# Kernel optimization log

Hardware: AMD Instinct MI355X
Metric: run time of the kernel (lower is better)

Reference implementation:

```python
import jax, jax.numpy as jnp
import numpy as np

MAX_DISP = 4  # matches init_kwargs


def setup_inputs() -> dict:
    key = jax.random.key(0)
    k1, k2 = jax.random.split(key)
    fmap1 = jax.random.normal(k1, (8, 256, 64, 128), dtype=jnp.float32)
    fmap2 = jax.random.normal(k2, (8, 256, 64, 128), dtype=jnp.float32)
    return {"fmap1": fmap1, "fmap2": fmap2}


def reference(fmap1, fmap2):
    # corr(x,y,dx,dy) = sum_c fmap1[c,y,x] * fmap2[c,y+dy,x+dx]
    pad = MAX_DISP
    B, C, H, W = fmap1.shape
    f2p = jnp.pad(fmap2, ((0, 0), (0, 0), (pad, pad), (pad, pad)))
    side = 2 * pad + 1  # 9 -> 81 displacements total
    # Loop over the small fixed set of 81 static displacements; each term is a
    # fused elementwise-multiply + channel reduction (einsum over c).
    corrs = [
        jnp.einsum('bchw,bchw->bhw', fmap1, f2p[:, :, y0:y0 + H, x0:x0 + W])
        for y0 in range(side)
        for x0 in range(side)
    ]
    return jnp.stack(corrs, axis=1)  # (B, 81, H, W)
```

## Files before the change

kernel.cpp:

```cpp
#include <hip/hip_runtime.h>


namespace {
constexpr int B_ = 8, C_ = 256, H_ = 64, W_ = 128;
constexpr int SIDE = 9, ND = 81, PAD = 4;
constexpr int HW = H_ * W_;
constexpr int KC = 32, NCH = C_ / KC;
constexpr int YB = 8, RWS = YB + 2 * PAD;
constexpr int XB = 16;
constexpr int NQ = 4;
constexpr int YP_ = H_ + 2 * PAD;
constexpr int XP_ = 144;
constexpr size_t ROWU = (size_t)NQ * XP_;
constexpr size_t PERB = (size_t)NCH * YP_ * ROWU;
constexpr size_t NW2 = (size_t)B_ * PERB;
constexpr size_t WS_BYTES = NW2 * 16;
constexpr int TILE_U4 = RWS * NQ * 32;
}

typedef __attribute__((ext_vector_type(8))) short short8;
typedef __attribute__((ext_vector_type(4))) float float4v;
typedef __attribute__((address_space(1))) void gvoid;
typedef __attribute__((address_space(3))) void svoid;

__device__ __forceinline__ unsigned bf16rne(float f) {
  unsigned u = __float_as_uint(f);
  return (u + 0x7fffu + ((u >> 16) & 1u)) >> 16;
}
__device__ __forceinline__ unsigned packbf2(float lo, float hi) {
  return bf16rne(lo) | (bf16rne(hi) << 16);
}

__global__ __launch_bounds__(256)
void cvt_f2(const float* __restrict__ f2, uint4* __restrict__ w2) {
  const int id = blockIdx.x;
  const int b = id & 7;
  const int e = (id >> 3) * 256 + (int)threadIdx.x;
  const int xp = e % XP_;
  int r = e / XP_;
  const int q = r & 3;
  r >>= 2;
  const int yp = r % YP_;
  const int cs = r / YP_;
  const int yg = yp - PAD, xg = xp - PAD;
  uint4 o = {0u, 0u, 0u, 0u};
  if (yg >= 0 && yg < H_ && xg >= 0 && xg < W_) {
    const float* s = f2 + ((size_t)(b * C_ + cs * KC + q * 8) * H_ + yg) * W_ + xg;
    o.x = packbf2(s[0 * HW], s[1 * HW]);
    o.y = packbf2(s[2 * HW], s[3 * HW]);
    o.z = packbf2(s[4 * HW], s[5 * HW]);
    o.w = packbf2(s[6 * HW], s[7 * HW]);
  }
  w2[(size_t)b * PERB + e] = o;
}

__global__ __launch_bounds__(512, 4)
void corr_mfma2(const float* __restrict__ f1, const uint4* __restrict__ w2,
                float* __restrict__ out) {
  __shared__ uint4 f2s[2 * TILE_U4];

  const int id = blockIdx.x;
  const int b = id & 7;
  const int k = id >> 3;
  const int xg = k & 7, yg = k >> 3;
  const int x0 = xg * XB, y0 = yg * YB;

  const int t = threadIdx.x, lane = t & 63, w = t >> 6;
  const int v = lane & 15, q = lane >> 4;
  const int sq = q << 1;
  const int l_hi = lane >> 5;
  const int l_xq = lane & 31;

  const uint4* w2b = w2 + (size_t)b * PERB;
  const float* f1b = f1 + (size_t)b * C_ * HW;

  auto issue_stage = [&](int ch, int buf) {
    const uint4* wc = w2b + (size_t)ch * ((size_t)YP_ * ROWU);
#pragma unroll
    for (int kk = 0; kk < 4; ++kk) {
      const int r = 2 * w + (kk >> 1);
      const int qp = kk & 1;
      const int qq = 2 * qp + l_hi;
      const int xqs = l_xq ^ (qq << 1);
      const uint4* gp = wc + (size_t)(y0 + r) * ROWU + (size_t)qq * XP_ + x0 + xqs;
      uint4* lp = &f2s[buf * TILE_U4 + (r * NQ + qp * 2) * 32];
      __builtin_amdgcn_global_load_lds((gvoid*)gp, (svoid*)lp, 16, 0, 0);
    }
  };
  auto issue_f1 = [&](int ch, float* p) {
    const float* fp =
        f1b + ((size_t)(ch * KC + q * 8) * H_ + (y0 + w)) * W_ + x0 + v;
#pragma unroll
    for (int j = 0; j < 8; ++j) p[j] = fp[(size_t)j * HW];
  };

  float4v acc[SIDE][2];
#pragma unroll
  for (int i = 0; i < SIDE; ++i) {
    acc[i][0] = (float4v){0.f, 0.f, 0.f, 0.f};
    acc[i][1] = (float4v){0.f, 0.f, 0.f, 0.f};
  }

  float p0[8], p1[8];
  issue_stage(0, 0);
  __builtin_amdgcn_sched_barrier(0);
  issue_f1(0, p0);
  __builtin_amdgcn_sched_barrier(0);
  issue_stage(1, 1);
  __builtin_amdgcn_sched_barrier(0);

#pragma unroll
  for (int ch = 0; ch < NCH; ++ch) {
    float* pc = (ch & 1) ? p1 : p0;
    uint4 afu;
    afu.x = packbf2(pc[0], pc[1]);
    afu.y = packbf2(pc[2], pc[3]);
    afu.z = packbf2(pc[4], pc[5]);
    afu.w = packbf2(pc[6], pc[7]);
    const short8 af = __builtin_bit_cast(short8, afu);

    asm volatile("s_waitcnt vmcnt(4)" ::: "memory");
    __builtin_amdgcn_s_barrier();
    __builtin_amdgcn_sched_barrier(0);

    if (ch + 1 < NCH) issue_f1(ch + 1, (ch & 1) ? p0 : p1);

    const int bo = (ch & 1) * TILE_U4;
#pragma unroll
    for (int dy = 0; dy < SIDE; ++dy) {
      const uint4* base = &f2s[bo + ((w + dy) * NQ + q) * 32];
      const short8 b0 = __builtin_bit_cast(short8, base[v ^ sq]);
      const short8 b1 = __builtin_bit_cast(short8, base[(v + 16) ^ sq]);
      acc[dy][0] =
          __builtin_amdgcn_mfma_f32_16x16x32_bf16(af, b0, acc[dy][0], 0, 0, 0);
      acc[dy][1] =
          __builtin_amdgcn_mfma_f32_16x16x32_bf16(af, b1, acc[dy][1], 0, 0, 0);
    }
    __builtin_amdgcn_sched_barrier(0);
    __builtin_amdgcn_s_barrier();
    __builtin_amdgcn_sched_barrier(0);
    if (ch + 2 < NCH) issue_stage(ch + 2, ch & 1);
  }

  const int y = y0 + w;
  float* outb = out + (size_t)b * ND * HW + (size_t)y * W_ + x0;
#pragma unroll
  for (int dy = 0; dy < SIDE; ++dy) {
#pragma unroll
    for (int r = 0; r < 4; ++r) {
      const int m = q * 4 + r;
      const int dx0 = v - m;
      if (dx0 >= 0 && dx0 <= 8)
        outb[(size_t)(dy * SIDE + dx0) * HW + m] = acc[dy][0][r];
      const int dx1 = v - m + 16;
      if (dx1 <= 8)
        outb[(size_t)(dy * SIDE + dx1) * HW + m] = acc[dy][1][r];
    }
  }
}

namespace fb {
constexpr int PXS = 20, F2PX = 32, F2U = 16 * (F2PX / 4) * 16;
}

__global__ __launch_bounds__(512, 4)
void corr_fb(const float* __restrict__ f1, const float* __restrict__ f2,
             float* __restrict__ out) {
  using namespace fb;
  __shared__ __align__(16) unsigned f2s[RWS * F2PX * PXS];
  __shared__ __align__(16) unsigned f1s[YB * XB * PXS];

  const int id = blockIdx.x;
  const int b = id & 7;
  const int k = id >> 3;
  const int xg = k & 7, yg = k >> 3;
  const int x0 = xg * XB, y0 = yg * YB;
  const int t = threadIdx.x, lane = t & 63, w = t >> 6;
  const int v = lane & 15, q = lane >> 4;

  float4v acc[SIDE][2];
#pragma unroll
  for (int i = 0; i < SIDE; ++i) {
    acc[i][0] = (float4v){0.f, 0.f, 0.f, 0.f};
    acc[i][1] = (float4v){0.f, 0.f, 0.f, 0.f};
  }
  const float* __restrict__ f1b = f1 + (size_t)b * C_ * HW;
  const float* __restrict__ f2b = f2 + (size_t)b * C_ * HW;

  for (int ch = 0; ch < NCH; ++ch) {
    const int c0 = ch * KC;
    if (ch) __syncthreads();
#pragma unroll
    for (int u0 = 0; u0 < F2U; u0 += 512) {
      const int u = u0 + t;
      const int cp = u & 15;
      const int t2 = u >> 4;
      const int pxq = t2 & 7;
      const int r = t2 >> 3;
      const int ygl = y0 - PAD + r;
      const int xb = x0 - PAD + pxq * 4;
      float4 va = make_float4(0.f, 0.f, 0.f, 0.f), vb = va;
      if (ygl >= 0 && ygl < H_ && xb >= 0 && xb <= W_ - 4) {
        const float* p = f2b + ((size_t)(c0 + 2 * cp) * H_ + ygl) * W_ + xb;
        va = *(const float4*)p;
        vb = *(const float4*)(p + HW);
      }
      unsigned* d = &f2s[(r * F2PX + pxq * 4) * PXS + cp];
      d[0 * PXS] = packbf2(va.x, vb.x);
      d[1 * PXS] = packbf2(va.y, vb.y);
      d[2 * PXS] = packbf2(va.z, vb.z);
      d[3 * PXS] = packbf2(va.w, vb.w);
    }
    {
      const int cp = t & 15;
      const int t2 = t >> 4;
      const int pxq = t2 & 3;
      const int r = t2 >> 2;
      const float* p =
          f1b + ((size_t)(c0 + 2 * cp) * H_ + (y0 + r)) * W_ + x0 + pxq * 4;
      const float4 va = *(const float4*)p;
      const float4 vb = *(const float4*)(p + HW);
      unsigned* d = &f1s[(r * XB + pxq * 4) * PXS + cp];
      d[0 * PXS] = packbf2(va.x, vb.x);
      d[1 * PXS] = packbf2(va.y, vb.y);
      d[2 * PXS] = packbf2(va.z, vb.z);
      d[3 * PXS] = packbf2(va.w, vb.w);
    }
    __syncthreads();

    const short8 af = __builtin_bit_cast(
        short8, *(const uint4*)&f1s[(w * XB + v) * PXS + 4 * q]);
#pragma unroll
    for (int dy = 0; dy < SIDE; ++dy) {
      const unsigned* fp = &f2s[((w + dy) * F2PX + v) * PXS + 4 * q];
      const short8 b0 = __builtin_bit_cast(short8, *(const uint4*)fp);
      const short8 b1 =
          __builtin_bit_cast(short8, *(const uint4*)(fp + 16 * PXS));
      acc[dy][0] =
          __builtin_amdgcn_mfma_f32_16x16x32_bf16(af, b0, acc[dy][0], 0, 0, 0);
      acc[dy][1] =
          __builtin_amdgcn_mfma_f32_16x16x32_bf16(af, b1, acc[dy][1], 0, 0, 0);
    }
  }
  const int y = y0 + w;
  float* outb = out + (size_t)b * ND * HW + (size_t)y * W_ + x0;
#pragma unroll
  for (int dy = 0; dy < SIDE; ++dy) {
#pragma unroll
    for (int r = 0; r < 4; ++r) {
      const int m = q * 4 + r;
      const int dx0 = v - m;
      if (dx0 >= 0 && dx0 <= 8)
        outb[(size_t)(dy * SIDE + dx0) * HW + m] = acc[dy][0][r];
      const int dx1 = v - m + 16;
      if (dx1 <= 8)
        outb[(size_t)(dy * SIDE + dx1) * HW + m] = acc[dy][1][r];
    }
  }
}

extern "C" void kernel_launch(void* const* d_in, const int* in_sizes, int n_in,
                              void* d_out, int out_size, void* d_ws,
                              size_t ws_size, hipStream_t stream) {
  (void)in_sizes; (void)n_in; (void)out_size;
  const float* f1 = (const float*)d_in[0];
  const float* f2 = (const float*)d_in[1];
  float* out = (float*)d_out;
  if (ws_size >= WS_BYTES) {
    uint4* w2 = (uint4*)d_ws;
    cvt_f2<<<dim3((unsigned)(NW2 / 256)), 256, 0, stream>>>(f2, w2);
    corr_mfma2<<<dim3(512), 512, 0, stream>>>(f1, w2, out);
  } else {
    corr_fb<<<dim3(512), 512, 0, stream>>>(f1, f2, out);
  }
}
```

Measured before the change: 182.6 us.

## Deepen fmap1 prefetch to triple buffer and vectorize bf16 conversion kernel

The conversion kernel now handles two x positions per thread, using float2 loads and writing two uint4 outputs, and launches half as many blocks. The main MFMA kernel prefetches fmap1 two chunks ahead with a three-slot register buffer. The waitcnt is relaxed to match the extra loads in flight, and wave priority is raised around the MFMA loop. The aim is to hide global-load latency for fmap1 and cut conversion-kernel instruction overhead, at the cost of more registers and possible occupancy pressure.

```diff
diff --git a/kernel.cpp b/kernel.cpp
--- a/kernel.cpp
+++ b/kernel.cpp
@@ -35,23 +35,36 @@
 void cvt_f2(const float* __restrict__ f2, uint4* __restrict__ w2) {
   const int id = blockIdx.x;
   const int b = id & 7;
-  const int e = (id >> 3) * 256 + (int)threadIdx.x;
-  const int xp = e % XP_;
-  int r = e / XP_;
+  const int e2 = (id >> 3) * 256 + (int)threadIdx.x;
+  const int xp2 = e2 % (XP_ / 2);
+  int r = e2 / (XP_ / 2);
   const int q = r & 3;
   r >>= 2;
   const int yp = r % YP_;
   const int cs = r / YP_;
+  const int xp = 2 * xp2;
   const int yg = yp - PAD, xg = xp - PAD;
-  uint4 o = {0u, 0u, 0u, 0u};
-  if (yg >= 0 && yg < H_ && xg >= 0 && xg < W_) {
-    const float* s = f2 + ((size_t)(b * C_ + cs * KC + q * 8) * H_ + yg) * W_ + xg;
-    o.x = packbf2(s[0 * HW], s[1 * HW]);
-    o.y = packbf2(s[2 * HW], s[3 * HW]);
-    o.z = packbf2(s[4 * HW], s[5 * HW]);
-    o.w = packbf2(s[6 * HW], s[7 * HW]);
-  }
-  w2[(size_t)b * PERB + e] = o;
+  uint4 o0 = {0u, 0u, 0u, 0u}, o1 = o0;
+  if (yg >= 0 && yg < H_ && xg >= 0 && xg <= W_ - 2) {
+    const float* s =
+        f2 + ((size_t)(b * C_ + cs * KC + q * 8) * H_ + yg) * W_ + xg;
+    const float2 v0 = *(const float2*)(s + 0 * HW);
+    const float2 v1 = *(const float2*)(s + 1 * HW);
+    const float2 v2 = *(const float2*)(s + 2 * HW);
+    const float2 v3 = *(const float2*)(s + 3 * HW);
+    const float2 v4 = *(const float2*)(s + 4 * HW);
+    const float2 v5 = *(const float2*)(s + 5 * HW);
+    const float2 v6 = *(const float2*)(s + 6 * HW);
+    const float2 v7 = *(const float2*)(s + 7 * HW);
+    o0.x = packbf2(v0.x, v1.x);  o1.x = packbf2(v0.y, v1.y);
+    o0.y = packbf2(v2.x, v3.x);  o1.y = packbf2(v2.y, v3.y);
+    o0.z = packbf2(v4.x, v5.x);  o1.z = packbf2(v4.y, v5.y);
+    o0.w = packbf2(v6.x, v7.x);  o1.w = packbf2(v6.y, v7.y);
+  }
+  const size_t e = (((size_t)(cs * YP_ + yp) * NQ + q) * XP_) + xp;
+  uint4* d = w2 + (size_t)b * PERB + e;
+  d[0] = o0;
+  d[1] = o1;
 }
 
 __global__ __launch_bounds__(512, 4)
@@ -101,17 +114,19 @@
     acc[i][1] = (float4v){0.f, 0.f, 0.f, 0.f};
   }
 
-  float p0[8], p1[8];
+  float pbuf[3][8];
   issue_stage(0, 0);
   __builtin_amdgcn_sched_barrier(0);
-  issue_f1(0, p0);
+  issue_f1(0, pbuf[0]);
   __builtin_amdgcn_sched_barrier(0);
   issue_stage(1, 1);
   __builtin_amdgcn_sched_barrier(0);
+  issue_f1(1, pbuf[1]);
+  __builtin_amdgcn_sched_barrier(0);
 
 #pragma unroll
   for (int ch = 0; ch < NCH; ++ch) {
-    float* pc = (ch & 1) ? p1 : p0;
+    float* pc = pbuf[ch % 3];
     uint4 afu;
     afu.x = packbf2(pc[0], pc[1]);
     afu.y = packbf2(pc[2], pc[3]);
@@ -119,13 +134,13 @@
     afu.w = packbf2(pc[6], pc[7]);
     const short8 af = __builtin_bit_cast(short8, afu);
 
-    asm volatile("s_waitcnt vmcnt(4)" ::: "memory");
+    asm volatile("s_waitcnt vmcnt(12)" ::: "memory");
+    __builtin_amdgcn_sched_barrier(0);
     __builtin_amdgcn_s_barrier();
     __builtin_amdgcn_sched_barrier(0);
 
-    if (ch + 1 < NCH) issue_f1(ch + 1, (ch & 1) ? p0 : p1);
-
     const int bo = (ch & 1) * TILE_U4;
+    __builtin_amdgcn_s_setprio(1);
 #pragma unroll
     for (int dy = 0; dy < SIDE; ++dy) {
       const uint4* base = &f2s[bo + ((w + dy) * NQ + q) * 32];
@@ -136,10 +151,16 @@
       acc[dy][1] =
           __builtin_amdgcn_mfma_f32_16x16x32_bf16(af, b1, acc[dy][1], 0, 0, 0);
     }
+    __builtin_amdgcn_s_setprio(0);
     __builtin_amdgcn_sched_barrier(0);
     __builtin_amdgcn_s_barrier();
     __builtin_amdgcn_sched_barrier(0);
-    if (ch + 2 < NCH) issue_stage(ch + 2, ch & 1);
+    if (ch + 2 < NCH) {
+      issue_stage(ch + 2, ch & 1);
+      __builtin_amdgcn_sched_barrier(0);
+      issue_f1(ch + 2, pbuf[(ch + 2) % 3]);
+      __builtin_amdgcn_sched_barrier(0);
+    }
   }
 
   const int y = y0 + w;
@@ -268,7 +289,7 @@
   float* out = (float*)d_out;
   if (ws_size >= WS_BYTES) {
     uint4* w2 = (uint4*)d_ws;
-    cvt_f2<<<dim3((unsigned)(NW2 / 256)), 256, 0, stream>>>(f2, w2);
+    cvt_f2<<<dim3((unsigned)(NW2 / 512)), 256, 0, stream>>>(f2, w2);
     corr_mfma2<<<dim3(512), 512, 0, stream>>>(f1, w2, out);
   } else {
     corr_fb<<<dim3(512), 512, 0, stream>>>(f1, f2, out);
```

Result: no change. 183.0 us (+0.2%).
